# Performance work log

Measured on AMD Instinct MI355X. Metric: run time of the kernel, lower is better.

Reference implementation:

```python
import jax, jax.numpy as jnp
from jax import lax
import numpy as np

N, R, WM, HM = 512, 64, 6, 6        # batch, n_rooms, padded room width/height
E, MX, MY = 16, 32, 24              # embedding width, map dims (from source)
MAP_CH = [32, 64, 64]; KS = [5, 3, 3]
ROOM_CH = [64, 64]; OUT = 64


def _boundaries(m):
    # faithful translation of _compute_room_boundaries (numpy, static room data)
    left = np.zeros_like(m); left[0] = m[0]; left[1:] = np.clip(m[1:] - m[:-1], 0, None)
    right = np.zeros_like(m); right[-1] = m[-1]; right[:-1] = np.clip(m[:-1] - m[1:], 0, None)
    up = np.zeros_like(m); up[:, 0] = m[:, 0]; up[:, 1:] = np.clip(m[:, 1:] - m[:, :-1], 0, None)
    down = np.zeros_like(m); down[:, -1] = m[:, -1]; down[:, :-1] = np.clip(m[:, :-1] - m[:, 1:], 0, None)
    return np.stack([left, right, up, down], 0)


def _make_rooms(rng):
    # synthetic Crateria-like rooms: [R, 9, WM, HM] = map, 4 door masks, 4 boundaries
    rooms = np.zeros((R, 9, WM, HM), np.float32)
    for i in range(R):
        w = int(rng.integers(2, WM + 1)); h = int(rng.integers(2, HM + 1))
        m = np.zeros((WM, HM), np.float32); m[:w, :h] = 1.0
        doors = (rng.random((4, WM, HM)) < 0.2).astype(np.float32) * m
        rooms[i] = np.concatenate([m[None], doors, _boundaries(m)], 0)
    return rooms


def setup_inputs():
    rng = np.random.default_rng(0)
    rooms = jnp.asarray(_make_rooms(rng))
    key = jax.random.key(0)
    ks = jax.random.split(key, 16)
    px = jax.random.randint(ks[0], (N, R, 1), 0, MX - WM + 1)
    py = jax.random.randint(ks[1], (N, R, 1), 0, MY - HM + 1)
    room_positions = jnp.concatenate([px, py], -1).astype(jnp.int32)
    emb = jax.random.normal(ks[2], (R, E), jnp.float32)
    cw = [10 + E] + MAP_CH
    inp = {"room_positions": room_positions, "rooms": rooms, "emb": emb}
    for i, k in enumerate(KS):
        inp[f"w{i}"] = jax.random.normal(ks[3 + i], (cw[i + 1], cw[i], k, k), jnp.float32) / np.float32(np.sqrt(cw[i] * k * k))
        inp[f"b{i}"] = jnp.zeros((cw[i + 1],), jnp.float32)
    rc = [MAP_CH[-1]] + ROOM_CH + [OUT]
    for i in range(3):
        inp[f"rw{i}"] = jax.random.normal(ks[8 + i], (rc[i + 1], rc[i]), jnp.float32) / np.float32(np.sqrt(rc[i]))
        inp[f"rb{i}"] = jnp.zeros((rc[i + 1],), jnp.float32)
    return inp


def _forward(room_positions, rooms, emb, w0, b0, w1, b1, w2, b2, rw0, rb0, rw1, rb1, rw2, rb2):
    n = room_positions.shape[0]
    # linearized scatter/gather indices for all rooms at once: [n, R*WM*HM]
    idx_x = room_positions[:, :, 0:1] + jnp.arange(WM)  # [n,R,WM]
    idx_y = room_positions[:, :, 1:2] + jnp.arange(HM)  # [n,R,HM]
    lin = (idx_x[:, :, :, None] * MY + idx_y[:, :, None, :]).reshape(n, R * WM * HM)
    vals9 = rooms.transpose(1, 0, 2, 3).reshape(9, R * WM * HM)
    valsE = (emb.T[:, :, None, None] * rooms[:, 0][None]).reshape(E, R * WM * HM)

    def scat(lin_i):
        fm = jnp.zeros((9, MX * MY), rooms.dtype).at[:, lin_i].add(vals9)
        em = jnp.zeros((E, MX * MY), rooms.dtype).at[:, lin_i].add(valsE)
        return fm, em

    fm, em = jax.vmap(scat)(lin)
    bg = jnp.ones((n, 1, MX * MY), rooms.dtype)  # channel 9 = 1.0 background
    X = jnp.concatenate([fm, bg, em], 1).reshape(n, 10 + E, MX, MY)
    # SAME-padded Conv2d + ReLU stack
    for w, b, k in ((w0, b0, KS[0]), (w1, b1, KS[1]), (w2, b2, KS[2])):
        p = k // 2
        X = lax.conv_general_dilated(X, w, (1, 1), [(p, p), (p, p)],
                                     dimension_numbers=("NCHW", "OIHW", "NCHW"))
        X = jax.nn.relu(X + b[None, :, None, None])
    # decode_map: gather each room's patch, mask by room map, sum spatially -> [n,C,R]
    C = X.shape[1]
    Xf = X.reshape(n, C, MX * MY)
    g = jax.vmap(lambda xi, li: xi[:, li])(Xf, lin).reshape(n, C, R, WM, HM)
    Y = (g * rooms[:, 0][None, None]).sum((3, 4))
    # 1x1 Conv1d head (pointwise over channels)
    Y = jax.nn.relu(jnp.einsum("oc,ncr->nor", rw0, Y) + rb0[None, :, None])
    Y = jax.nn.relu(jnp.einsum("oc,ncr->nor", rw1, Y) + rb1[None, :, None])
    Y = jnp.einsum("oc,ncr->nor", rw2, Y) + rb2[None, :, None]
    return Y.transpose(0, 2, 1)  # [n, R, output_width]


def reference(room_positions, rooms, emb, w0, b0, w1, b1, w2, b2, rw0, rb0, rw1, rb1, rw2, rb2):
    return _forward(room_positions, rooms, emb, w0, b0, w1, b1, w2, b2,
                    rw0, rb0, rw1, rb1, rw2, rb2)
```

## Files before the change

### kernel.cpp

```cpp
#include <hip/hip_runtime.h>
#include <hip/hip_bf16.h>
#include <stdint.h>

typedef short v8s __attribute__((ext_vector_type(8)));
typedef float v4f __attribute__((ext_vector_type(4)));

#define TPB 1024

#define X0_OFF 0
#define X1_OFF 106496
#define X2_OFF 0
#define X3_OFF 106496
#define YA_OFF 0
#define YB_OFF 16384
#define EMB_OFF 57344
#define MK_OFF 159744
#define CH8_OFF 160256
#define RPL_OFF 162560
#define MW_OFF 163072
#define SMEM_BYTES 163520

#define WS0_U 0
#define WS1_U 3200
#define WS2_U 5504
#define WS_UNITS 10112

__device__ __forceinline__ uint16_t f2b(float f) {
    __hip_bfloat16 h = __float2bfloat16(f);
    return *reinterpret_cast<uint16_t*>(&h);
}
__device__ __forceinline__ uint32_t pkbf(float lo, float hi) {
    return (uint32_t)f2b(lo) | ((uint32_t)f2b(hi) << 16);
}
__device__ __forceinline__ float b2f(uint16_t h) {
    return __uint_as_float(((uint32_t)h) << 16);
}

__global__ void prep_weights(const float* __restrict__ w0,
                             const float* __restrict__ w1,
                             const float* __restrict__ w2,
                             uint8_t* __restrict__ ws)
{
    int u = blockIdx.x * 256 + threadIdx.x;
    if (u >= WS_UNITS) return;
    int l = u & 63, fid = u >> 6;
    const float* src; int IC, KS_, t, kf, m;
    if (fid < 50)      { src = w0; IC = 26; KS_ = 5; t = fid >> 1; kf = 0; m = fid & 1; }
    else if (fid < 86) { int v = fid - 50; src = w1; IC = 32; KS_ = 3; t = v >> 2; kf = 0; m = v & 3; }
    else               { int v = fid - 86; src = w2; IC = 64; KS_ = 3; t = v >> 3; kf = (v >> 2) & 1; m = v & 3; }
    int oc = m * 16 + (l & 15);
    int kb = kf * 32 + ((l >> 4) * 8);
    int ky = t / KS_, kx = t - ky * KS_;
    v8s out;
#pragma unroll
    for (int j = 0; j < 8; ++j) {
        int k = kb + j;
        float v = (k < IC) ? src[((oc * IC + k) * KS_ + ky) * KS_ + kx] : 0.f;
        out[j] = (short)f2b(v);
    }
    ((v8s*)ws)[u] = out;
}

template<int MT, int KF, int TAPS, int KS, int PAD,
         int IN_OFF, int IN_SH, int IN_ROWS, int WS_BASE, int MT_TOT>
__device__ __forceinline__ void conv_core(const uint8_t* smem, const v8s* __restrict__ wsv,
                                          int l, const int* px, const int* py,
                                          v4f (&acc)[MT][3])
{
    const int kgoff = ((l >> 4) << 4);
    constexpr int MSK = (IN_SH == 7) ? 7 : 3;
    for (int t = 0; t < TAPS; ++t) {
        const int ky = t / KS, kx = t - ky * KS;
        const int dx = ky - PAD, dy = kx - PAD;
        v8s af[MT][KF];
#pragma unroll
        for (int m = 0; m < MT; ++m)
#pragma unroll
            for (int kf = 0; kf < KF; ++kf)
                af[m][kf] = wsv[WS_BASE + ((t * KF + kf) * MT_TOT + m) * 64 + l];
#pragma unroll
        for (int i = 0; i < 3; ++i) {
            const int xi = px[i] + dx;
            const int rowp = xi * IN_ROWS + py[i] + dy + PAD;
            int a = ((rowp << IN_SH) | kgoff) ^ ((rowp & MSK) << 4);
            a = ((unsigned)xi < 32u) ? a : kgoff;
            a += IN_OFF;
            const v8s bf0 = *(const v8s*)(smem + a);
#pragma unroll
            for (int m = 0; m < MT; ++m)
                acc[m][i] = __builtin_amdgcn_mfma_f32_16x16x32_bf16(af[m][0], bf0, acc[m][i], 0, 0, 0);
            if (KF == 2) {
                const v8s bf1 = *(const v8s*)(smem + (a ^ 64));
#pragma unroll
                for (int m = 0; m < MT; ++m)
                    acc[m][i] = __builtin_amdgcn_mfma_f32_16x16x32_bf16(af[m][1], bf1, acc[m][i], 0, 0, 0);
            }
        }
    }
}

template<int MTOT, int M0, int M1, int OUT_OFF, int OUT_SH, int OUT_ROWS, int OUT_PAD>
__device__ __forceinline__ void conv_epi(uint8_t* smem, const float* __restrict__ bias,
                                         v4f (&acc)[MTOT][3], const int* px, const int* py, int kg)
{
    constexpr int MSK = (OUT_SH == 7) ? 7 : 3;
#pragma unroll
    for (int m = M0; m < M1; ++m) {
        const float* bp = bias + m * 16 + kg * 4;
        const float bb0 = bp[0], bb1 = bp[1], bb2 = bp[2], bb3 = bp[3];
#pragma unroll
        for (int i = 0; i < 3; ++i) {
            const float v0 = fmaxf(acc[m][i][0] + bb0, 0.f);
            const float v1 = fmaxf(acc[m][i][1] + bb1, 0.f);
            const float v2 = fmaxf(acc[m][i][2] + bb2, 0.f);
            const float v3 = fmaxf(acc[m][i][3] + bb3, 0.f);
            uint2 pk;
            pk.x = pkbf(v0, v1);
            pk.y = pkbf(v2, v3);
            const int rowp = px[i] * OUT_ROWS + py[i] + OUT_PAD;
            const int coff = (m - M0) * 32 + (kg << 3);
            const int a = OUT_OFF + (((rowp << OUT_SH) | coff) ^ ((rowp & MSK) << 4));
            *(uint2*)(smem + a) = pk;
        }
    }
}

__device__ __forceinline__ void gather_half(const uint8_t* smem,
                                            const uint32_t* __restrict__ mk,
                                            const int* __restrict__ rpl,
                                            int gr, int gl, float* yreg)
{
    const int pxr = rpl[gr * 2], pyr = rpl[gr * 2 + 1];
    const uint32_t mlo = mk[gr * 2], mhi = mk[gr * 2 + 1];
    float s0=0,s1=0,s2=0,s3=0,s4=0,s5=0,s6=0,s7=0;
#pragma unroll
    for (int cell = 0; cell < 36; ++cell) {
        const uint32_t w = (cell < 32) ? mlo : mhi;
        if ((w >> (cell & 31)) & 1u) {
            const int p = (pxr + cell / 6) * 24 + pyr + (cell % 6);
            const v8s v = *(const v8s*)(smem + X3_OFF +
                (((p << 6) | (gl << 4)) ^ ((p & 3) << 4)));
            s0 += b2f((uint16_t)v[0]);
            s1 += b2f((uint16_t)v[1]);
            s2 += b2f((uint16_t)v[2]);
            s3 += b2f((uint16_t)v[3]);
            s4 += b2f((uint16_t)v[4]);
            s5 += b2f((uint16_t)v[5]);
            s6 += b2f((uint16_t)v[6]);
            s7 += b2f((uint16_t)v[7]);
        }
    }
    yreg[0]=s0; yreg[1]=s1; yreg[2]=s2; yreg[3]=s3;
    yreg[4]=s4; yreg[5]=s5; yreg[6]=s6; yreg[7]=s7;
}

template<bool RELU>
__device__ __forceinline__ void mlp_layer(uint8_t* smem, int inoff, int outoff,
                                          const float* __restrict__ W,
                                          const float* __restrict__ bias, int tid)
{
    const int og = tid >> 6, r = tid & 63;
    const int ogs = __builtin_amdgcn_readfirstlane(og);
    const int swz = (r & 7) << 4;
    float acc[4];
#pragma unroll
    for (int oo = 0; oo < 4; ++oo) acc[oo] = bias[ogs * 4 + oo];
    const float* Wb = W + ogs * 4 * 64;
#pragma unroll
    for (int cg = 0; cg < 16; ++cg) {
        const v4f v = *(const v4f*)(smem + inoff + ((r * 256 + cg * 16) ^ swz));
#pragma unroll
        for (int oo = 0; oo < 4; ++oo) {
            const float* wr = Wb + oo * 64 + cg * 4;
            acc[oo] = fmaf(wr[0], v[0], acc[oo]);
            acc[oo] = fmaf(wr[1], v[1], acc[oo]);
            acc[oo] = fmaf(wr[2], v[2], acc[oo]);
            acc[oo] = fmaf(wr[3], v[3], acc[oo]);
        }
    }
    if (RELU)
#pragma unroll
        for (int oo = 0; oo < 4; ++oo) acc[oo] = fmaxf(acc[oo], 0.f);
    const v4f o0 = {acc[0], acc[1], acc[2], acc[3]};
    *(v4f*)(smem + outoff + ((r * 256 + ogs * 16) ^ swz)) = o0;
}

__global__ __launch_bounds__(TPB)
void fused_main(const int* __restrict__ rpos,
                const float* __restrict__ rooms,
                const float* __restrict__ emb,
                const float* __restrict__ b0, const float* __restrict__ b1,
                const float* __restrict__ b2,
                const float* __restrict__ rw0, const float* __restrict__ rb0,
                const float* __restrict__ rw1, const float* __restrict__ rb1,
                const float* __restrict__ rw2, const float* __restrict__ rb2,
                const uint8_t* __restrict__ ws,
                float* __restrict__ out)
{
    __shared__ __align__(16) uint8_t smem[SMEM_BYTES];
    const int tid = threadIdx.x, n = blockIdx.x;
    const int* rp = rpos + n * 128;
    const v8s* wsv = (const v8s*)ws;
    uint32_t* mk  = (uint32_t*)(smem + MK_OFF);
    uint8_t*  ch8 = smem + CH8_OFF;
    int*      rpl = (int*)(smem + RPL_OFF);
    uint32_t* mw  = (uint32_t*)(smem + MW_OFF);
    float*    embl = (float*)(smem + EMB_OFF);

    embl[tid] = emb[tid];
    if (tid < 112) mw[tid] = 0;
    if (tid >= 128 && tid < 256) mk[tid - 128] = 0;
    if (tid >= 256 && tid < 384) rpl[tid - 256] = rp[tid - 256];
    __syncthreads();
    if (tid < 64) {
        const int pxr = rpl[2 * tid], pyr = rpl[2 * tid + 1];
        const uint32_t bit = 1u << (tid & 31);
        const int xb = (tid >> 5) * 32, yb = 64 + (tid >> 5) * 24;
#pragma unroll
        for (int i = 0; i < 6; ++i) atomicOr(&mw[xb + pxr + i], bit);
#pragma unroll
        for (int j = 0; j < 6; ++j) atomicOr(&mw[yb + pyr + j], bit);
    }
    for (int q = tid; q < 2304; q += TPB) {
        const int r = (q * 1821) >> 16;
        const int cell = q - r * 36;
        const float* base = rooms + r * 324 + cell;
        uint32_t bits = 0;
#pragma unroll
        for (int c = 1; c < 9; ++c)
            bits |= (base[c * 36] != 0.f ? 1u : 0u) << (c - 1);
        ch8[q] = (uint8_t)bits;
        if (base[0] != 0.f) atomicOr(&mk[r * 2 + (cell >> 5)], 1u << (cell & 31));
    }
    __syncthreads();

    if (tid < 768) {
        const int x = (tid * 2731) >> 16;
        const int y = tid - x * 24;
        float a[26];
#pragma unroll
        for (int c = 0; c < 26; ++c) a[c] = 0.f;
        a[9] = 1.f;
        uint32_t mlo = mw[x] & mw[64 + y];
        uint32_t mhi = mw[32 + x] & mw[88 + y];
#pragma unroll 1
        for (int half = 0; half < 2; ++half) {
            uint32_t mm = half ? mhi : mlo;
            const int rb = half ? 32 : 0;
            while (mm) {
                const int r = rb + __builtin_ctz(mm);
                mm &= mm - 1;
                const int cell = (x - rpl[2 * r]) * 6 + (y - rpl[2 * r + 1]);
                const uint32_t w = mk[r * 2 + (cell >> 5)];
                if ((w >> (cell & 31)) & 1u) {
                    a[0] += 1.f;
                    const uint32_t bits = ch8[r * 36 + cell];
#pragma unroll
                    for (int c = 0; c < 8; ++c)
                        a[1 + c] += (float)((bits >> c) & 1u);
                    const float* er = embl + r * 16;
#pragma unroll
                    for (int e = 0; e < 16; ++e) a[10 + e] += er[e];
                }
            }
        }
        const int row = x * 28 + y + 2;
        const int swz = (row & 3) << 4;
#pragma unroll
        for (int cg = 0; cg < 4; ++cg) {
            float c[8];
#pragma unroll
            for (int j = 0; j < 8; ++j) {
                const int ci = cg * 8 + j;
                c[j] = (ci < 26) ? a[(ci < 26) ? ci : 0] : 0.f;
            }
            uint2 p0, p1;
            p0.x = pkbf(c[0], c[1]); p0.y = pkbf(c[2], c[3]);
            p1.x = pkbf(c[4], c[5]); p1.y = pkbf(c[6], c[7]);
            const int a0 = X0_OFF + (((row << 6) | (cg << 4)) ^ swz);
            *(uint2*)(smem + a0)     = p0;
            *(uint2*)(smem + a0 + 8) = p1;
        }
    } else {
        const int base = (tid - 768) * 2;
#pragma unroll
        for (int k = 0; k < 2; ++k) {
            const int u = base + k;
            const int rowi = u >> 2, slot = u & 3;
            const int x = rowi >> 2, yp = rowi & 3;
            const int row = x * 28 + ((yp < 2) ? yp : yp + 24);
            *(v8s*)(smem + X0_OFF + (((row << 6) | (slot << 4)) ^ ((row & 3) << 4))) =
                (v8s){0,0,0,0,0,0,0,0};
        }
    }
    __syncthreads();

    const int l = tid & 63, wv = tid >> 6, kg = l >> 4;
    int px[3], py[3];
#pragma unroll
    for (int i = 0; i < 3; ++i) {
        const int p = (wv + 16 * i) * 16 + (l & 15);
        const int x = (p * 2731) >> 16;
        px[i] = x; py[i] = p - x * 24;
    }

    {
        if (tid < 256) {
            const int rowi = tid >> 2, slot = tid & 3;
            const int x = rowi >> 1;
            const int rowp = x * 26 + ((rowi & 1) ? 25 : 0);
            *(v8s*)(smem + X1_OFF + (((rowp << 6) | (slot << 4)) ^ ((rowp & 3) << 4))) =
                (v8s){0,0,0,0,0,0,0,0};
        }
        v4f acc[2][3];
#pragma unroll
        for (int m = 0; m < 2; ++m)
#pragma unroll
            for (int i = 0; i < 3; ++i) acc[m][i] = (v4f){0.f,0.f,0.f,0.f};
        conv_core<2,1,25,5,2, X0_OFF,6,28, WS0_U,2>(smem, wsv, l, px, py, acc);
        conv_epi<2,0,2, X1_OFF,6,26,1>(smem, b0, acc, px, py, kg);
    }
    __syncthreads();

    {
        if (tid < 512) {
            const int rowi = tid >> 3, slot = tid & 7;
            const int x = rowi >> 1;
            const int rowp = x * 26 + ((rowi & 1) ? 25 : 0);
            *(v8s*)(smem + X2_OFF + (((rowp << 7) | (slot << 4)) ^ ((rowp & 7) << 4))) =
                (v8s){0,0,0,0,0,0,0,0};
        }
        v4f acc[4][3];
#pragma unroll
        for (int m = 0; m < 4; ++m)
#pragma unroll
            for (int i = 0; i < 3; ++i) acc[m][i] = (v4f){0.f,0.f,0.f,0.f};
        conv_core<4,1,9,3,1, X1_OFF,6,26, WS1_U,4>(smem, wsv, l, px, py, acc);
        conv_epi<4,0,4, X2_OFF,7,26,1>(smem, b1, acc, px, py, kg);
    }
    __syncthreads();

    float yregA[8], yregB[8];
    {
        v4f acc[4][3];
#pragma unroll
        for (int m = 0; m < 4; ++m)
#pragma unroll
            for (int i = 0; i < 3; ++i) acc[m][i] = (v4f){0.f,0.f,0.f,0.f};
        conv_core<4,2,9,3,1, X2_OFF,7,26, WS2_U,4>(smem, wsv, l, px, py, acc);
        conv_epi<4,0,2, X3_OFF,6,24,0>(smem, b2, acc, px, py, kg);
        __syncthreads();
        if (tid < 256) gather_half(smem, mk, rpl, tid >> 2, tid & 3, yregA);
        __syncthreads();
        conv_epi<4,2,4, X3_OFF,6,24,0>(smem, b2, acc, px, py, kg);
        __syncthreads();
        if (tid < 256) gather_half(smem, mk, rpl, tid >> 2, tid & 3, yregB);
        __syncthreads();
    }

    if (tid < 256) {
        const int gr = tid >> 2, gl = tid & 3;
        const int swz = (gr & 7) << 4;
        const int baseA = gr * 256 + gl * 32;
        const int baseB = baseA + 128;
        *(v4f*)(smem + YA_OFF + (baseA ^ swz))        = (v4f){yregA[0], yregA[1], yregA[2], yregA[3]};
        *(v4f*)(smem + YA_OFF + ((baseA + 16) ^ swz)) = (v4f){yregA[4], yregA[5], yregA[6], yregA[7]};
        *(v4f*)(smem + YA_OFF + (baseB ^ swz))        = (v4f){yregB[0], yregB[1], yregB[2], yregB[3]};
        *(v4f*)(smem + YA_OFF + ((baseB + 16) ^ swz)) = (v4f){yregB[4], yregB[5], yregB[6], yregB[7]};
    }
    __syncthreads();

    mlp_layer<true >(smem, YA_OFF, YB_OFF, rw0, rb0, tid);
    __syncthreads();
    mlp_layer<true >(smem, YB_OFF, YA_OFF, rw1, rb1, tid);
    __syncthreads();
    mlp_layer<false>(smem, YA_OFF, YB_OFF, rw2, rb2, tid);
    __syncthreads();

    {
        const int r = tid >> 4, cg = tid & 15;
        const int swz = (r & 7) << 4;
        const v4f v = *(const v4f*)(smem + YB_OFF + ((r * 256 + cg * 16) ^ swz));
        *(v4f*)(out + n * 4096 + r * 64 + cg * 4) = v;
    }
}

extern "C" void kernel_launch(void* const* d_in, const int* in_sizes, int n_in,
                              void* d_out, int out_size, void* d_ws, size_t ws_size,
                              hipStream_t stream) {
    const int*   rpos  = (const int*)  d_in[0];
    const float* rooms = (const float*)d_in[1];
    const float* emb   = (const float*)d_in[2];
    const float* w0    = (const float*)d_in[3];
    const float* b0    = (const float*)d_in[4];
    const float* w1    = (const float*)d_in[5];
    const float* b1    = (const float*)d_in[6];
    const float* w2    = (const float*)d_in[7];
    const float* b2    = (const float*)d_in[8];
    const float* rw0   = (const float*)d_in[9];
    const float* rb0   = (const float*)d_in[10];
    const float* rw1   = (const float*)d_in[11];
    const float* rb1   = (const float*)d_in[12];
    const float* rw2   = (const float*)d_in[13];
    const float* rb2   = (const float*)d_in[14];
    float* out = (float*)d_out;
    uint8_t* ws = (uint8_t*)d_ws;

    const int n = in_sizes[0] / 128;
    hipLaunchKernelGGL(prep_weights, dim3((WS_UNITS + 255) / 256), dim3(256), 0, stream,
                       w0, w1, w2, ws);
    hipLaunchKernelGGL(fused_main, dim3(n), dim3(TPB), 0, stream,
                       rpos, rooms, emb, b0, b1, b2,
                       rw0, rb0, rw1, rb1, rw2, rb2, ws, out);
}
```

Before: 114.1 us.

## Write full conv2 output once and gather rooms in a single pass

The final conv layer now writes all 64 output channels into a repurposed shared-memory region in one epilogue, instead of two 32-channel halves each followed by a gather pass. The room gather then runs once with 512 threads, 8 channels each, and writes straight into the MLP input buffer. This removes two barriers and one gather pass. The input-building stage also recomputes the room loop once per 8-channel group, so fewer accumulators stay live (lower register pressure) at the cost of repeating the mask walk four times.

```diff
diff --git a/kernel.cpp b/kernel.cpp
--- a/kernel.cpp
+++ b/kernel.cpp
@@ -10,9 +10,9 @@
 #define X0_OFF 0
 #define X1_OFF 106496
 #define X2_OFF 0
-#define X3_OFF 106496
-#define YA_OFF 0
-#define YB_OFF 16384
+#define X3_OFF 0
+#define YA_OFF 106496
+#define YB_OFF 122880
 #define EMB_OFF 57344
 #define MK_OFF 159744
 #define CH8_OFF 160256
@@ -125,35 +125,6 @@
     }
 }
 
-__device__ __forceinline__ void gather_half(const uint8_t* smem,
-                                            const uint32_t* __restrict__ mk,
-                                            const int* __restrict__ rpl,
-                                            int gr, int gl, float* yreg)
-{
-    const int pxr = rpl[gr * 2], pyr = rpl[gr * 2 + 1];
-    const uint32_t mlo = mk[gr * 2], mhi = mk[gr * 2 + 1];
-    float s0=0,s1=0,s2=0,s3=0,s4=0,s5=0,s6=0,s7=0;
-#pragma unroll
-    for (int cell = 0; cell < 36; ++cell) {
-        const uint32_t w = (cell < 32) ? mlo : mhi;
-        if ((w >> (cell & 31)) & 1u) {
-            const int p = (pxr + cell / 6) * 24 + pyr + (cell % 6);
-            const v8s v = *(const v8s*)(smem + X3_OFF +
-                (((p << 6) | (gl << 4)) ^ ((p & 3) << 4)));
-            s0 += b2f((uint16_t)v[0]);
-            s1 += b2f((uint16_t)v[1]);
-            s2 += b2f((uint16_t)v[2]);
-            s3 += b2f((uint16_t)v[3]);
-            s4 += b2f((uint16_t)v[4]);
-            s5 += b2f((uint16_t)v[5]);
-            s6 += b2f((uint16_t)v[6]);
-            s7 += b2f((uint16_t)v[7]);
-        }
-    }
-    yreg[0]=s0; yreg[1]=s1; yreg[2]=s2; yreg[3]=s3;
-    yreg[4]=s4; yreg[5]=s5; yreg[6]=s6; yreg[7]=s7;
-}
-
 template<bool RELU>
 __device__ __forceinline__ void mlp_layer(uint8_t* smem, int inoff, int outoff,
                                           const float* __restrict__ W,
@@ -237,46 +208,42 @@
     if (tid < 768) {
         const int x = (tid * 2731) >> 16;
         const int y = tid - x * 24;
-        float a[26];
-#pragma unroll
-        for (int c = 0; c < 26; ++c) a[c] = 0.f;
-        a[9] = 1.f;
-        uint32_t mlo = mw[x] & mw[64 + y];
-        uint32_t mhi = mw[32 + x] & mw[88 + y];
+        const uint32_t mlo = mw[x] & mw[64 + y];
+        const uint32_t mhi = mw[32 + x] & mw[88 + y];
+        const int row = x * 28 + y + 2;
+        const int swz = (row & 3) << 4;
+#pragma unroll
+        for (int cg = 0; cg < 4; ++cg) {
+            float a8[8];
+#pragma unroll
+            for (int j = 0; j < 8; ++j) a8[j] = 0.f;
+            if (cg == 1) a8[1] = 1.f;
 #pragma unroll 1
-        for (int half = 0; half < 2; ++half) {
-            uint32_t mm = half ? mhi : mlo;
-            const int rb = half ? 32 : 0;
-            while (mm) {
-                const int r = rb + __builtin_ctz(mm);
-                mm &= mm - 1;
-                const int cell = (x - rpl[2 * r]) * 6 + (y - rpl[2 * r + 1]);
-                const uint32_t w = mk[r * 2 + (cell >> 5)];
-                if ((w >> (cell & 31)) & 1u) {
-                    a[0] += 1.f;
-                    const uint32_t bits = ch8[r * 36 + cell];
-#pragma unroll
-                    for (int c = 0; c < 8; ++c)
-                        a[1 + c] += (float)((bits >> c) & 1u);
-                    const float* er = embl + r * 16;
-#pragma unroll
-                    for (int e = 0; e < 16; ++e) a[10 + e] += er[e];
+            for (int half = 0; half < 2; ++half) {
+                uint32_t mm = half ? mhi : mlo;
+                const int rb = half ? 32 : 0;
+                while (mm) {
+                    const int r = rb + __builtin_ctz(mm);
+                    mm &= mm - 1;
+                    const int cell = (x - rpl[2 * r]) * 6 + (y - rpl[2 * r + 1]);
+                    const uint32_t w = mk[r * 2 + (cell >> 5)];
+                    if ((w >> (cell & 31)) & 1u) {
+                        const uint32_t bits = ch8[r * 36 + cell];
+                        const float* er = embl + r * 16;
+#pragma unroll
+                        for (int j = 0; j < 8; ++j) {
+                            const int c = cg * 8 + j;
+                            if (c == 0)       a8[j] += 1.f;
+                            else if (c <= 8)  a8[j] += (float)((bits >> (c - 1)) & 1u);
+                            else if (c == 9)  {  }
+                            else if (c < 26)  a8[j] += er[c - 10];
+                        }
+                    }
                 }
             }
-        }
-        const int row = x * 28 + y + 2;
-        const int swz = (row & 3) << 4;
-#pragma unroll
-        for (int cg = 0; cg < 4; ++cg) {
-            float c[8];
-#pragma unroll
-            for (int j = 0; j < 8; ++j) {
-                const int ci = cg * 8 + j;
-                c[j] = (ci < 26) ? a[(ci < 26) ? ci : 0] : 0.f;
-            }
             uint2 p0, p1;
-            p0.x = pkbf(c[0], c[1]); p0.y = pkbf(c[2], c[3]);
-            p1.x = pkbf(c[4], c[5]); p1.y = pkbf(c[6], c[7]);
+            p0.x = pkbf(a8[0], a8[1]); p0.y = pkbf(a8[2], a8[3]);
+            p1.x = pkbf(a8[4], a8[5]); p1.y = pkbf(a8[6], a8[7]);
             const int a0 = X0_OFF + (((row << 6) | (cg << 4)) ^ swz);
             *(uint2*)(smem + a0)     = p0;
             *(uint2*)(smem + a0 + 8) = p1;
@@ -340,7 +307,6 @@
     }
     __syncthreads();
 
-    float yregA[8], yregB[8];
     {
         v4f acc[4][3];
 #pragma unroll
@@ -348,25 +314,36 @@
 #pragma unroll
             for (int i = 0; i < 3; ++i) acc[m][i] = (v4f){0.f,0.f,0.f,0.f};
         conv_core<4,2,9,3,1, X2_OFF,7,26, WS2_U,4>(smem, wsv, l, px, py, acc);
-        conv_epi<4,0,2, X3_OFF,6,24,0>(smem, b2, acc, px, py, kg);
         __syncthreads();
-        if (tid < 256) gather_half(smem, mk, rpl, tid >> 2, tid & 3, yregA);
+        conv_epi<4,0,4, X3_OFF,7,24,0>(smem, b2, acc, px, py, kg);
         __syncthreads();
-        conv_epi<4,2,4, X3_OFF,6,24,0>(smem, b2, acc, px, py, kg);
-        __syncthreads();
-        if (tid < 256) gather_half(smem, mk, rpl, tid >> 2, tid & 3, yregB);
-        __syncthreads();
-    }
-
-    if (tid < 256) {
-        const int gr = tid >> 2, gl = tid & 3;
+    }
+    if (tid < 512) {
+        const int gr = tid >> 3, gg = tid & 7;
+        const int pxr = rpl[gr * 2], pyr = rpl[gr * 2 + 1];
+        const uint32_t mlo = mk[gr * 2], mhi = mk[gr * 2 + 1];
+        float s0=0,s1=0,s2=0,s3=0,s4=0,s5=0,s6=0,s7=0;
+#pragma unroll
+        for (int cell = 0; cell < 36; ++cell) {
+            const uint32_t w = (cell < 32) ? mlo : mhi;
+            if ((w >> (cell & 31)) & 1u) {
+                const int p = (pxr + cell / 6) * 24 + pyr + (cell % 6);
+                const v8s v = *(const v8s*)(smem + X3_OFF +
+                    (((p << 7) | (gg << 4)) ^ ((p & 7) << 4)));
+                s0 += b2f((uint16_t)v[0]);
+                s1 += b2f((uint16_t)v[1]);
+                s2 += b2f((uint16_t)v[2]);
+                s3 += b2f((uint16_t)v[3]);
+                s4 += b2f((uint16_t)v[4]);
+                s5 += b2f((uint16_t)v[5]);
+                s6 += b2f((uint16_t)v[6]);
+                s7 += b2f((uint16_t)v[7]);
+            }
+        }
+        const int base = gr * 256 + gg * 32;
         const int swz = (gr & 7) << 4;
-        const int baseA = gr * 256 + gl * 32;
-        const int baseB = baseA + 128;
-        *(v4f*)(smem + YA_OFF + (baseA ^ swz))        = (v4f){yregA[0], yregA[1], yregA[2], yregA[3]};
-        *(v4f*)(smem + YA_OFF + ((baseA + 16) ^ swz)) = (v4f){yregA[4], yregA[5], yregA[6], yregA[7]};
-        *(v4f*)(smem + YA_OFF + (baseB ^ swz))        = (v4f){yregB[0], yregB[1], yregB[2], yregB[3]};
-        *(v4f*)(smem + YA_OFF + ((baseB + 16) ^ swz)) = (v4f){yregB[4], yregB[5], yregB[6], yregB[7]};
+        *(v4f*)(smem + YA_OFF + (base ^ swz))        = (v4f){s0, s1, s2, s3};
+        *(v4f*)(smem + YA_OFF + ((base + 16) ^ swz)) = (v4f){s4, s5, s6, s7};
     }
     __syncthreads();
 
```

New measurement: 129.6 us. 13.6% more time.

## Pad X0 rows to 80-byte stride and split conv2 K-fragments into two passes

Applied to the files above, without the earlier changes.

Layer 0's input buffer moves from a 64-byte XOR-swizzled row layout to an unswizzled 80-byte row stride, presumably to avoid LDS bank conflicts in a different way. EMB_OFF is relocated so it does not overlap the larger X0 region. conv_core is generalised to take a byte stride, an optional swizzle mask and a single K-fragment selector. Conv layer 2 now runs as two sequential passes over the taps, one per 32-channel half, which lowers live weight-fragment registers but doubles the loop overhead and repeats the address computation.

```diff
diff --git a/kernel.cpp b/kernel.cpp
--- a/kernel.cpp
+++ b/kernel.cpp
@@ -8,12 +8,12 @@
 #define TPB 1024
 
 #define X0_OFF 0
+#define EMB_OFF 73728
 #define X1_OFF 106496
 #define X2_OFF 0
 #define X3_OFF 106496
 #define YA_OFF 0
 #define YB_OFF 16384
-#define EMB_OFF 57344
 #define MK_OFF 159744
 #define CH8_OFF 160256
 #define RPL_OFF 162560
@@ -61,40 +61,32 @@
     ((v8s*)ws)[u] = out;
 }
 
-template<int MT, int KF, int TAPS, int KS, int PAD,
-         int IN_OFF, int IN_SH, int IN_ROWS, int WS_BASE, int MT_TOT>
+template<int MT, int FRAGK, int KSEL, int TAPS, int KS, int PAD,
+         int IN_OFF, int IN_STRIDE, int IN_MSK, int IN_ROWS, int WS_BASE, int MT_TOT>
 __device__ __forceinline__ void conv_core(const uint8_t* smem, const v8s* __restrict__ wsv,
                                           int l, const int* px, const int* py,
                                           v4f (&acc)[MT][3])
 {
-    const int kgoff = ((l >> 4) << 4);
-    constexpr int MSK = (IN_SH == 7) ? 7 : 3;
+    const int kgoff = ((l >> 4) << 4) + KSEL * 64;
     for (int t = 0; t < TAPS; ++t) {
         const int ky = t / KS, kx = t - ky * KS;
         const int dx = ky - PAD, dy = kx - PAD;
-        v8s af[MT][KF];
+        v8s af[MT];
 #pragma unroll
         for (int m = 0; m < MT; ++m)
-#pragma unroll
-            for (int kf = 0; kf < KF; ++kf)
-                af[m][kf] = wsv[WS_BASE + ((t * KF + kf) * MT_TOT + m) * 64 + l];
+            af[m] = wsv[WS_BASE + ((t * FRAGK + KSEL) * MT_TOT + m) * 64 + l];
 #pragma unroll
         for (int i = 0; i < 3; ++i) {
             const int xi = px[i] + dx;
             const int rowp = xi * IN_ROWS + py[i] + dy + PAD;
-            int a = ((rowp << IN_SH) | kgoff) ^ ((rowp & MSK) << 4);
+            int a = rowp * IN_STRIDE + kgoff;
+            if (IN_MSK) a ^= (rowp & IN_MSK) << 4;
             a = ((unsigned)xi < 32u) ? a : kgoff;
             a += IN_OFF;
-            const v8s bf0 = *(const v8s*)(smem + a);
+            const v8s bf = *(const v8s*)(smem + a);
 #pragma unroll
             for (int m = 0; m < MT; ++m)
-                acc[m][i] = __builtin_amdgcn_mfma_f32_16x16x32_bf16(af[m][0], bf0, acc[m][i], 0, 0, 0);
-            if (KF == 2) {
-                const v8s bf1 = *(const v8s*)(smem + (a ^ 64));
-#pragma unroll
-                for (int m = 0; m < MT; ++m)
-                    acc[m][i] = __builtin_amdgcn_mfma_f32_16x16x32_bf16(af[m][1], bf1, acc[m][i], 0, 0, 0);
-            }
+                acc[m][i] = __builtin_amdgcn_mfma_f32_16x16x32_bf16(af[m], bf, acc[m][i], 0, 0, 0);
         }
     }
 }
@@ -265,7 +257,6 @@
             }
         }
         const int row = x * 28 + y + 2;
-        const int swz = (row & 3) << 4;
 #pragma unroll
         for (int cg = 0; cg < 4; ++cg) {
             float c[8];
@@ -277,7 +268,7 @@
             uint2 p0, p1;
             p0.x = pkbf(c[0], c[1]); p0.y = pkbf(c[2], c[3]);
             p1.x = pkbf(c[4], c[5]); p1.y = pkbf(c[6], c[7]);
-            const int a0 = X0_OFF + (((row << 6) | (cg << 4)) ^ swz);
+            const int a0 = X0_OFF + row * 80 + cg * 16;
             *(uint2*)(smem + a0)     = p0;
             *(uint2*)(smem + a0 + 8) = p1;
         }
@@ -289,8 +280,7 @@
             const int rowi = u >> 2, slot = u & 3;
             const int x = rowi >> 2, yp = rowi & 3;
             const int row = x * 28 + ((yp < 2) ? yp : yp + 24);
-            *(v8s*)(smem + X0_OFF + (((row << 6) | (slot << 4)) ^ ((row & 3) << 4))) =
-                (v8s){0,0,0,0,0,0,0,0};
+            *(v8s*)(smem + X0_OFF + row * 80 + slot * 16) = (v8s){0,0,0,0,0,0,0,0};
         }
     }
     __syncthreads();
@@ -317,7 +307,7 @@
         for (int m = 0; m < 2; ++m)
 #pragma unroll
             for (int i = 0; i < 3; ++i) acc[m][i] = (v4f){0.f,0.f,0.f,0.f};
-        conv_core<2,1,25,5,2, X0_OFF,6,28, WS0_U,2>(smem, wsv, l, px, py, acc);
+        conv_core<2,1,0,25,5,2, X0_OFF,80,0,28, WS0_U,2>(smem, wsv, l, px, py, acc);
         conv_epi<2,0,2, X1_OFF,6,26,1>(smem, b0, acc, px, py, kg);
     }
     __syncthreads();
@@ -335,7 +325,7 @@
         for (int m = 0; m < 4; ++m)
 #pragma unroll
             for (int i = 0; i < 3; ++i) acc[m][i] = (v4f){0.f,0.f,0.f,0.f};
-        conv_core<4,1,9,3,1, X1_OFF,6,26, WS1_U,4>(smem, wsv, l, px, py, acc);
+        conv_core<4,1,0,9,3,1, X1_OFF,64,3,26, WS1_U,4>(smem, wsv, l, px, py, acc);
         conv_epi<4,0,4, X2_OFF,7,26,1>(smem, b1, acc, px, py, kg);
     }
     __syncthreads();
@@ -347,7 +337,8 @@
         for (int m = 0; m < 4; ++m)
 #pragma unroll
             for (int i = 0; i < 3; ++i) acc[m][i] = (v4f){0.f,0.f,0.f,0.f};
-        conv_core<4,2,9,3,1, X2_OFF,7,26, WS2_U,4>(smem, wsv, l, px, py, acc);
+        conv_core<4,2,0,9,3,1, X2_OFF,128,7,26, WS2_U,4>(smem, wsv, l, px, py, acc);
+        conv_core<4,2,1,9,3,1, X2_OFF,128,7,26, WS2_U,4>(smem, wsv, l, px, py, acc);
         conv_epi<4,0,2, X3_OFF,6,24,0>(smem, b2, acc, px, py, kg);
         __syncthreads();
         if (tid < 256) gather_half(smem, mk, rpl, tid >> 2, tid & 3, yregA);
```

After: 149.0 us. 1.31x slower.
